# Optimization experiments

Hardware: AMD Instinct MI355X
Metric: run time of the kernel (lower is better)

Reference implementation:

```python
import jax, jax.numpy as jnp
import numpy as np

C = 64          # channels
N = 4096        # number of sampled coords (64x64 grid)
SPACING = (0.001, 0.001)
SHIFT = jnp.array([SPACING[0] / 2.0, SPACING[1] / 2.0], dtype=jnp.float32)  # 'nearest' mode shift


def setup_inputs() -> dict:
    key = jax.random.key(0)
    k1, k2 = jax.random.split(key)
    values = jax.random.normal(k1, (C, N), dtype=jnp.float32)
    coords = jax.random.uniform(k2, (N, 2), dtype=jnp.float32)
    return {"values": values, "coords": coords}


def reference(values, coords):
    """upsample_nn, mode='nearest', grid_mode=True, scale=4.
    values: [C, N], coords: [N, 2] -> output [C, 4N]."""
    sx, sy = SPACING
    x, y = coords[:, 0], coords[:, 1]
    # three shifted copies of the grid -> [3N, 2]
    new_coords = jnp.concatenate([
        jnp.stack([x, y + sy], axis=1),
        jnp.stack([x + sx, y], axis=1),
        jnp.stack([x + sx, y + sy], axis=1),
    ], axis=0)
    q = new_coords - SHIFT                                  # [3N, 2]
    # squared pairwise distances via expansion (argmin-equivalent to norm)
    d2 = (q * q).sum(1)[:, None] + (coords * coords).sum(1)[None, :] \
         - 2.0 * (q @ coords.T)                             # [3N, N]
    idx = jnp.argmin(d2, axis=1)                            # nearest old coord per new coord
    new_values = values[:, idx]                             # [C, 3N] irregular gather
    return jnp.concatenate([values, new_values], axis=1)    # [C, 4N]
```

## Files before the change

### kernel.cpp

```cpp
#include <hip/hip_runtime.h>


#pragma clang fp contract(off)

constexpr int   Nn    = 4096;
constexpr int   Cc    = 64;
constexpr int   NQ    = 3 * Nn;
constexpr int   GD    = 64;
constexpr int   NCELL = GD * GD;
constexpr float Rm    = 3.5e-3f;
constexpr int   QPB   = 64;
constexpr int   QBLK  = NQ / QPB;
constexpr int   NBLK  = QBLK + 64;

__global__ __launch_bounds__(256) void upsample_fused_kernel(
    const float* __restrict__ values,
    const float* __restrict__ coords,
    float* __restrict__ out)
{
#pragma clang fp contract(off)
    __shared__ float2         sC[Nn];
    __shared__ int            sCnt[NCELL];
    __shared__ unsigned short sSort[Nn];
    __shared__ int            sWave[4];
    __shared__ int            sBi[QPB];

    const int tid = threadIdx.x;

    if (blockIdx.x >= QBLK) {
        int b = blockIdx.x - QBLK;
        #pragma unroll
        for (int k = 0; k < 4; ++k) {
            int gi  = b * 1024 + k * 256 + tid;
            int row = gi >> 10;
            int c4  = gi & 1023;
            float4 v = reinterpret_cast<const float4*>(values)[row * 1024 + c4];
            reinterpret_cast<float4*>(out)[row * 4096 + c4] = v;
        }
        return;
    }

    #pragma unroll
    for (int k = 0; k < NCELL / 256; ++k) sCnt[tid + 256 * k] = 0;
    #pragma unroll
    for (int k = 0; k < Nn / 256; ++k) {
        int j = tid + 256 * k;
        sC[j] = reinterpret_cast<const float2*>(coords)[j];
    }
    __syncthreads();

    #pragma unroll
    for (int k = 0; k < Nn / 256; ++k) {
        int j = tid + 256 * k;
        float2 c = sC[j];
        int cx = min(GD - 1, (int)(c.x * (float)GD));
        int cy = min(GD - 1, (int)(c.y * (float)GD));
        atomicAdd(&sCnt[cy * GD + cx], 1);
    }
    __syncthreads();

    int loc[16];
    int run = 0;
    #pragma unroll
    for (int k = 0; k < 16; ++k) { loc[k] = run; run += sCnt[tid * 16 + k]; }
    const int lane = tid & 63, wid = tid >> 6;
    int inc = run;
    #pragma unroll
    for (int off = 1; off < 64; off <<= 1) {
        int nv = __shfl_up(inc, off, 64);
        if (lane >= off) inc += nv;
    }
    if (lane == 63) sWave[wid] = inc;
    __syncthreads();
    int woff = 0;
    #pragma unroll
    for (int w = 0; w < 4; ++w) if (w < wid) woff += sWave[w];
    const int texcl = woff + (inc - run);
    __syncthreads();
    #pragma unroll
    for (int k = 0; k < 16; ++k) sCnt[tid * 16 + k] = texcl + loc[k];
    __syncthreads();

    #pragma unroll
    for (int k = 0; k < Nn / 256; ++k) {
        int j = tid + 256 * k;
        float2 c = sC[j];
        int cx = min(GD - 1, (int)(c.x * (float)GD));
        int cy = min(GD - 1, (int)(c.y * (float)GD));
        int pos = atomicAdd(&sCnt[cy * GD + cx], 1);
        sSort[pos] = (unsigned short)j;
    }
    __syncthreads();

    if (tid < QPB) {
        const int q   = blockIdx.x * QPB + tid;
        const int i   = q & (Nn - 1);
        const int var = q >> 12;

        float2 ci = sC[i];
        const float x = ci.x, y = ci.y;
        float qx, qy;
        if (var == 0) {
            qx = x - 0.0005f;
            qy = (y + 0.001f) - 0.0005f;
        } else if (var == 1) {
            qx = (x + 0.001f) - 0.0005f;
            qy = y - 0.0005f;
        } else {
            qx = (x + 0.001f) - 0.0005f;
            qy = (y + 0.001f) - 0.0005f;
        }
        const float qq = qx * qx + qy * qy;

        const int xlo = max(0, (int)floorf((qx - Rm) * (float)GD));
        const int xhi = min(GD - 1, (int)floorf((qx + Rm) * (float)GD));
        const int ylo = max(0, (int)floorf((qy - Rm) * (float)GD));
        const int yhi = min(GD - 1, (int)floorf((qy + Rm) * (float)GD));

        float bd = INFINITY;
        int   bi = 0x7fffffff;
        for (int cy = ylo; cy <= yhi; ++cy) {
            int cellLo = cy * GD + xlo;
            int cellHi = cy * GD + xhi;
            int s = (cellLo == 0) ? 0 : sCnt[cellLo - 1];
            int e = sCnt[cellHi];
            for (int p = s; p < e; ++p) {
                int    jj = sSort[p];
                float2 c  = sC[jj];
                float  cc = c.x * c.x + c.y * c.y;
                float  qc = __builtin_fmaf(qy, c.y, qx * c.x);
                float  d2 = (qq + cc) - (qc + qc);
                if (d2 < bd || (d2 == bd && jj < bi)) { bd = d2; bi = jj; }
            }
        }
        sBi[tid] = bi;
    }
    __syncthreads();

    {
        const int ql = tid & 63;
        const int cg = tid >> 6;
        const int bi = sBi[ql];
        const int q0 = blockIdx.x * QPB;
        #pragma unroll
        for (int k = 0; k < 16; ++k) {
            int ch = cg * 16 + k;
            out[(size_t)ch * (4 * Nn) + Nn + q0 + ql] = values[ch * Nn + bi];
        }
    }
}

extern "C" void kernel_launch(void* const* d_in, const int* in_sizes, int n_in,
                              void* d_out, int out_size, void* d_ws, size_t ws_size,
                              hipStream_t stream) {
    const float* values = (const float*)d_in[0];
    const float* coords = (const float*)d_in[1];
    float* out = (float*)d_out;
    hipLaunchKernelGGL(upsample_fused_kernel, dim3(NBLK), dim3(256), 0, stream,
                       values, coords, out);
}
```

Measured before the change: 13.24 us.

## Coarsen grid, keep coords in registers, store sorted points directly, single-wave scan

Coarsens the spatial grid from 64x64 to 32x32 cells, so the 1024 cell counts can be prefix-scanned by a single wave without the cross-wave combine and its extra barriers. Coordinates are loaded as float4 into registers and the cell index is computed once, with no shared staging copy. Sorted point coordinates are written directly into shared memory alongside their ids, removing the indirect lookup in the search loop. The coarser cells mean each query scans more candidate points per cell, and register pressure goes up from holding 16 points and cells per thread.

After: 13.29 us. No clear change (+0.4%).

```diff
diff --git a/kernel.cpp b/kernel.cpp
--- a/kernel.cpp
+++ b/kernel.cpp
@@ -6,7 +6,7 @@
 constexpr int   Nn    = 4096;
 constexpr int   Cc    = 64;
 constexpr int   NQ    = 3 * Nn;
-constexpr int   GD    = 64;
+constexpr int   GD    = 32;
 constexpr int   NCELL = GD * GD;
 constexpr float Rm    = 3.5e-3f;
 constexpr int   QPB   = 64;
@@ -19,10 +19,9 @@
     float* __restrict__ out)
 {
 #pragma clang fp contract(off)
-    __shared__ float2         sC[Nn];
     __shared__ int            sCnt[NCELL];
-    __shared__ unsigned short sSort[Nn];
-    __shared__ int            sWave[4];
+    __shared__ float2         sPts[Nn];
+    __shared__ unsigned short sIds[Nn];
     __shared__ int            sBi[QPB];
 
     const int tid = threadIdx.x;
@@ -40,64 +39,61 @@
         return;
     }
 
+    const int q    = blockIdx.x * QPB + (tid & 63);
+    const int isrc = q & (Nn - 1);
+    float2 ci = make_float2(0.f, 0.f);
+    if (tid < QPB) ci = reinterpret_cast<const float2*>(coords)[isrc];
+
     #pragma unroll
     for (int k = 0; k < NCELL / 256; ++k) sCnt[tid + 256 * k] = 0;
+
+    float2 pt[16];
+    int    cell[16];
     #pragma unroll
-    for (int k = 0; k < Nn / 256; ++k) {
-        int j = tid + 256 * k;
-        sC[j] = reinterpret_cast<const float2*>(coords)[j];
+    for (int k = 0; k < 8; ++k) {
+        int t4 = tid + 256 * k;
+        float4 v = reinterpret_cast<const float4*>(coords)[t4];
+        pt[2 * k]     = make_float2(v.x, v.y);
+        pt[2 * k + 1] = make_float2(v.z, v.w);
+    }
+    __syncthreads();
+    #pragma unroll
+    for (int k = 0; k < 16; ++k) {
+        int cx = min(GD - 1, (int)(pt[k].x * (float)GD));
+        int cy = min(GD - 1, (int)(pt[k].y * (float)GD));
+        cell[k] = cy * GD + cx;
+        atomicAdd(&sCnt[cell[k]], 1);
+    }
+    __syncthreads();
+
+    if (tid < 64) {
+        int loc[16];
+        int run = 0;
+        #pragma unroll
+        for (int k = 0; k < 16; ++k) { loc[k] = run; run += sCnt[tid * 16 + k]; }
+        int inc = run;
+        #pragma unroll
+        for (int off = 1; off < 64; off <<= 1) {
+            int nv = __shfl_up(inc, off, 64);
+            if (tid >= off) inc += nv;
+        }
+        const int excl = inc - run;
+        #pragma unroll
+        for (int k = 0; k < 16; ++k) sCnt[tid * 16 + k] = excl + loc[k];
     }
     __syncthreads();
 
     #pragma unroll
-    for (int k = 0; k < Nn / 256; ++k) {
-        int j = tid + 256 * k;
-        float2 c = sC[j];
-        int cx = min(GD - 1, (int)(c.x * (float)GD));
-        int cy = min(GD - 1, (int)(c.y * (float)GD));
-        atomicAdd(&sCnt[cy * GD + cx], 1);
-    }
-    __syncthreads();
-
-    int loc[16];
-    int run = 0;
-    #pragma unroll
-    for (int k = 0; k < 16; ++k) { loc[k] = run; run += sCnt[tid * 16 + k]; }
-    const int lane = tid & 63, wid = tid >> 6;
-    int inc = run;
-    #pragma unroll
-    for (int off = 1; off < 64; off <<= 1) {
-        int nv = __shfl_up(inc, off, 64);
-        if (lane >= off) inc += nv;
-    }
-    if (lane == 63) sWave[wid] = inc;
-    __syncthreads();
-    int woff = 0;
-    #pragma unroll
-    for (int w = 0; w < 4; ++w) if (w < wid) woff += sWave[w];
-    const int texcl = woff + (inc - run);
-    __syncthreads();
-    #pragma unroll
-    for (int k = 0; k < 16; ++k) sCnt[tid * 16 + k] = texcl + loc[k];
-    __syncthreads();
-
-    #pragma unroll
-    for (int k = 0; k < Nn / 256; ++k) {
-        int j = tid + 256 * k;
-        float2 c = sC[j];
-        int cx = min(GD - 1, (int)(c.x * (float)GD));
-        int cy = min(GD - 1, (int)(c.y * (float)GD));
-        int pos = atomicAdd(&sCnt[cy * GD + cx], 1);
-        sSort[pos] = (unsigned short)j;
+    for (int k = 0; k < 16; ++k) {
+        int pos = atomicAdd(&sCnt[cell[k]], 1);
+        int j   = ((tid + 256 * (k >> 1)) << 1) | (k & 1);
+        sPts[pos] = pt[k];
+        sIds[pos] = (unsigned short)j;
     }
     __syncthreads();
 
     if (tid < QPB) {
-        const int q   = blockIdx.x * QPB + tid;
-        const int i   = q & (Nn - 1);
         const int var = q >> 12;
-
-        float2 ci = sC[i];
         const float x = ci.x, y = ci.y;
         float qx, qy;
         if (var == 0) {
@@ -125,8 +121,8 @@
             int s = (cellLo == 0) ? 0 : sCnt[cellLo - 1];
             int e = sCnt[cellHi];
             for (int p = s; p < e; ++p) {
-                int    jj = sSort[p];
-                float2 c  = sC[jj];
+                float2 c  = sPts[p];
+                int    jj = sIds[p];
                 float  cc = c.x * c.x + c.y * c.y;
                 float  qc = __builtin_fmaf(qy, c.y, qx * c.x);
                 float  d2 = (qq + cc) - (qc + qc);
```
